# Kernel optimization log

Measured on AMD Instinct MI355X. Metric: run time of the kernel, lower is better.

Reference implementation:

```python
import jax, jax.numpy as jnp
import numpy as np

N_CODES = 1024
DIM = 64
COMMITMENT = 0.25


def setup_inputs() -> dict:
    key = jax.random.key(0)
    k1, k2 = jax.random.split(key)
    z = jax.random.normal(k1, (32, DIM, 64, 64), dtype=jnp.float32)
    # nn.Embedding weight initialized uniform(-1/n_codes, 1/n_codes)
    codebook = jax.random.uniform(
        k2, (N_CODES, DIM), dtype=jnp.float32,
        minval=-1.0 / N_CODES, maxval=1.0 / N_CODES)
    return {"z": z, "codebook": codebook}


def reference(z, codebook):
    B, C, H, W = z.shape
    # (B,C,H,W) -> (B*H*W, C)
    z_flat = jnp.transpose(z, (0, 2, 3, 1)).reshape(-1, C)
    # squared L2 distances via expansion: |z|^2 + |e|^2 - 2 z.e
    dists = (
        jnp.sum(z_flat ** 2, axis=1, keepdims=True)
        + jnp.sum(codebook ** 2, axis=1)
        - 2.0 * z_flat @ codebook.T
    )  # [N, n_codes]
    indices = jnp.argmin(dists, axis=1)  # [N]
    z_q = jnp.transpose(codebook[indices].reshape(B, H, W, C), (0, 3, 1, 2))
    commit_loss = jnp.mean((jax.lax.stop_gradient(z_q) - z) ** 2)
    codebook_loss = jnp.mean((z_q - jax.lax.stop_gradient(z)) ** 2)
    vq_loss = codebook_loss + COMMITMENT * commit_loss
    z_q_st = z + jax.lax.stop_gradient(z_q - z)  # straight-through
    return (z_q_st, vq_loss)
```

## Files before the change

### kernel.cpp

```cpp
#include <hip/hip_runtime.h>


constexpr int DIM    = 64;
constexpr int NCODES = 1024;
constexpr int HWSZ   = 4096;
constexpr int NPOS   = 131072;
constexpr int BLOCK  = 1024;
constexpr int PPB    = 512;
constexpr int GRID   = NPOS / PPB;
constexpr int CIP    = 68;

typedef float    f32x4  __attribute__((ext_vector_type(4)));
typedef float    f32x2  __attribute__((ext_vector_type(2)));
typedef unsigned uint2v __attribute__((ext_vector_type(2)));
typedef unsigned uint4v __attribute__((ext_vector_type(4)));

__global__ __launch_bounds__(BLOCK, 4) void vq_all(const float* __restrict__ z,
                                                   const float* __restrict__ cb,
                                                   float* __restrict__ out) {
    __shared__ __align__(16) unsigned char cb_lds[NCODES * DIM];
    __shared__ float cinit_lds[16 * CIP];
    __shared__ int   bj_lds[PPB];
    __shared__ float ls_lds[BLOCK / 64];

    const int tid  = threadIdx.x;
    const int w    = tid >> 6;
    const int lane = tid & 63;
    const int q    = lane >> 4;
    const int r    = lane & 15;
    const int p0   = blockIdx.x * PPB;
    const int b    = p0 >> 12;
    const int hwb  = p0 & 4095;

    {
        const int j = tid;
        const float4* src = (const float4*)(cb + (size_t)j * DIM);
        unsigned words[16];
        float nq = 0.f;
#pragma unroll
        for (int g8 = 0; g8 < 8; g8++) {
            float4 v0 = src[g8 * 2], v1 = src[g8 * 2 + 1];
            int lo = 0, hi = 0;
            lo = __builtin_amdgcn_cvt_pk_fp8_f32(v0.x * 512.f, v0.y * 512.f, lo, 0);
            lo = __builtin_amdgcn_cvt_pk_fp8_f32(v0.z * 512.f, v0.w * 512.f, lo, 1);
            hi = __builtin_amdgcn_cvt_pk_fp8_f32(v1.x * 512.f, v1.y * 512.f, hi, 0);
            hi = __builtin_amdgcn_cvt_pk_fp8_f32(v1.z * 512.f, v1.w * 512.f, hi, 1);
            words[g8 * 2] = (unsigned)lo; words[g8 * 2 + 1] = (unsigned)hi;
#pragma unroll
            for (int m = 0; m < 2; m++) {
                int wv = m ? hi : lo;
                f32x2 d0 = __builtin_amdgcn_cvt_pk_f32_fp8(wv, 0);
                f32x2 d1 = __builtin_amdgcn_cvt_pk_f32_fp8(wv, 1);
                nq += d0[0] * d0[0] + d0[1] * d0[1] + d1[0] * d1[0] + d1[1] * d1[1];
            }
        }
        const int sswz = (j & 3) ^ ((j >> 2) & 1);
#pragma unroll
        for (int u = 0; u < 4; u++) {
            int us = u ^ sswz;
            uint4v tq = {words[2 * u], words[2 * u + 1],
                         words[2 * u + 8], words[2 * u + 9]};
            *(uint4v*)&cb_lds[(size_t)j * 64 + us * 16] = tq;
        }
        cinit_lds[(j & 15) * CIP + (j >> 4)] = 8.f - nq * (1.f / 1024.f);
    }

    long  afrag[2][2];
    float zsq[2];
#pragma unroll
    for (int s = 0; s < 2; s++) {
        const float* zb = z + (size_t)b * DIM * HWSZ + hwb + s * 256 + w * 16 + r;
        float sq = 0.f;
#pragma unroll
        for (int h = 0; h < 2; h++) {
            float v[8];
#pragma unroll
            for (int i = 0; i < 8; i++) {
                v[i] = zb[(size_t)(h * 32 + q * 8 + i) * HWSZ];
                sq = fmaf(v[i], v[i], sq);
            }
            int lo = 0, hi = 0;
            lo = __builtin_amdgcn_cvt_pk_fp8_f32(v[0], v[1], lo, 0);
            lo = __builtin_amdgcn_cvt_pk_fp8_f32(v[2], v[3], lo, 1);
            hi = __builtin_amdgcn_cvt_pk_fp8_f32(v[4], v[5], hi, 0);
            hi = __builtin_amdgcn_cvt_pk_fp8_f32(v[6], v[7], hi, 1);
            uint2v u = {(unsigned)lo, (unsigned)hi};
            afrag[s][h] = __builtin_bit_cast(long, u);
        }
        sq += __shfl_xor(sq, 16, 64);
        sq += __shfl_xor(sq, 32, 64);
        zsq[s] = sq;
    }

    __syncthreads();

    const int bbase = r * 64 + ((q ^ (r & 3) ^ ((r >> 2) & 1)) * 16);

    float best0[4], best1[4], tmp0[4], tmp1[4];
#pragma unroll
    for (int g = 0; g < 4; g++) { best0[g] = 0.f; best1[g] = 0.f; }

    uint4v Bp[4];
    Bp[0] = *(const uint4v*)&cb_lds[0 * 1024 + bbase];
    Bp[1] = *(const uint4v*)&cb_lds[1 * 1024 + bbase];
    Bp[2] = *(const uint4v*)&cb_lds[2 * 1024 + bbase];
    Bp[3] = *(const uint4v*)&cb_lds[3 * 1024 + bbase];
    float4 ci[2];
    ci[0] = *(const float4*)&cinit_lds[r * CIP + 0];
    ci[1] = *(const float4*)&cinit_lds[r * CIP + 4];

    f32x4 accR[3][2];

    auto ISSUE = [&](int jt) {
        const int slot = jt & 3;
        const float cin = ci[(jt >> 2) & 1][jt & 3];
        uint2v blo = {Bp[slot][0], Bp[slot][1]};
        uint2v bhi = {Bp[slot][2], Bp[slot][3]};
        f32x4 c0 = {cin, cin, cin, cin};
        f32x4 a0 = __builtin_amdgcn_mfma_f32_16x16x32_fp8_fp8(
            afrag[0][0], __builtin_bit_cast(long, blo), c0, 0, 0, 0);
        a0 = __builtin_amdgcn_mfma_f32_16x16x32_fp8_fp8(
            afrag[0][1], __builtin_bit_cast(long, bhi), a0, 0, 0, 0);
        f32x4 a1 = __builtin_amdgcn_mfma_f32_16x16x32_fp8_fp8(
            afrag[1][0], __builtin_bit_cast(long, blo), c0, 0, 0, 0);
        a1 = __builtin_amdgcn_mfma_f32_16x16x32_fp8_fp8(
            afrag[1][1], __builtin_bit_cast(long, bhi), a1, 0, 0, 0);
        accR[jt % 3][0] = a0;
        accR[jt % 3][1] = a1;
        Bp[slot] = *(const uint4v*)&cb_lds[(((jt + 4) & 63) * 1024) + bbase];
        if ((jt & 3) == 3)
            ci[(jt >> 2) & 1] =
                *(const float4*)&cinit_lds[r * CIP + ((((jt >> 2) + 2) & 15) * 4)];
    };

    auto PROCESS = [&](int pj) {
        const unsigned kk  = (unsigned)(1023 - pj * 16);
        const unsigned tag = kk - (unsigned)r;
#pragma unroll
        for (int g = 0; g < 4; g++) {
            unsigned bits0 = (__float_as_uint(accR[pj % 3][0][g]) & ~1023u)
                           | (tag & 1023u);
            unsigned bits1 = (__float_as_uint(accR[pj % 3][1][g]) & ~1023u)
                           | (tag & 1023u);
            float pf0 = __uint_as_float(bits0);
            float pf1 = __uint_as_float(bits1);
            if ((pj & 1) == 0) {
                tmp0[g] = pf0; tmp1[g] = pf1;
            } else {
                best0[g] = fmaxf(fmaxf(best0[g], tmp0[g]), pf0);
                best1[g] = fmaxf(fmaxf(best1[g], tmp1[g]), pf1);
            }
        }
    };

    ISSUE(0);
    ISSUE(1);
#pragma unroll
    for (int jt = 2; jt < 64; jt++) {
        ISSUE(jt);
        PROCESS(jt - 2);
    }
    PROCESS(62);
    PROCESS(63);

    unsigned bestu0[4], bestu1[4];
#pragma unroll
    for (int g = 0; g < 4; g++) {
        unsigned v0 = __float_as_uint(best0[g]);
        unsigned v1 = __float_as_uint(best1[g]);
#pragma unroll
        for (int off = 1; off < 16; off <<= 1) {
            unsigned w0 = __shfl_xor((int)v0, off, 64);
            unsigned w1 = __shfl_xor((int)v1, off, 64);
            v0 = v0 > w0 ? v0 : w0;
            v1 = v1 > w1 ? v1 : w1;
        }
        bestu0[g] = v0; bestu1[g] = v1;
    }

    float lsum = 0.f;
    if (q == (r >> 2)) {
        int g = r & 3;
        unsigned v0 = bestu0[0], v1 = bestu1[0];
        v0 = (g == 1) ? bestu0[1] : v0;  v1 = (g == 1) ? bestu1[1] : v1;
        v0 = (g == 2) ? bestu0[2] : v0;  v1 = (g == 2) ? bestu1[2] : v1;
        v0 = (g == 3) ? bestu0[3] : v0;  v1 = (g == 3) ? bestu1[3] : v1;
        bj_lds[w * 16 + r]       = 1023 - (int)(v0 & 1023u);
        bj_lds[256 + w * 16 + r] = 1023 - (int)(v1 & 1023u);
        lsum = zsq[0] + (8.f - __uint_as_float(v0)) * (1.f / 256.f)
             + zsq[1] + (8.f - __uint_as_float(v1)) * (1.f / 256.f);
    }
#pragma unroll
    for (int off = 32; off > 0; off >>= 1) lsum += __shfl_down(lsum, off, 64);
    if (lane == 0) ls_lds[w] = lsum;
    __syncthreads();
    if (tid == 0) {
        float s = 0.f;
#pragma unroll
        for (int i = 0; i < BLOCK / 64; i++) s += ls_lds[i];
        atomicAdd(out + (size_t)NPOS * DIM, s * (1.25f / 8388608.f));
    }

    int posi = tid & 511;
    int uu   = tid >> 9;
    int myj  = bj_lds[posi];
    int swzj = (myj & 3) ^ ((myj >> 2) & 1);
    float* ob = out + (size_t)b * DIM * HWSZ + hwb + posi;
#pragma unroll
    for (int k = 0; k < 2; k++) {
        int u  = uu + 2 * k;
        int us = u ^ swzj;
        uint4v t = *(const uint4v*)&cb_lds[(size_t)myj * 64 + us * 16];
#pragma unroll
        for (int m = 0; m < 2; m++) {
            int cbase = (m == 0) ? (8 * u) : (32 + 8 * u);
#pragma unroll
            for (int wd = 0; wd < 2; wd++) {
                int word = (int)t[m * 2 + wd];
                f32x2 d0 = __builtin_amdgcn_cvt_pk_f32_fp8(word, 0);
                f32x2 d1 = __builtin_amdgcn_cvt_pk_f32_fp8(word, 1);
                ob[(size_t)(cbase + wd * 4 + 0) * HWSZ] = d0[0] * (1.f / 512.f);
                ob[(size_t)(cbase + wd * 4 + 1) * HWSZ] = d0[1] * (1.f / 512.f);
                ob[(size_t)(cbase + wd * 4 + 2) * HWSZ] = d1[0] * (1.f / 512.f);
                ob[(size_t)(cbase + wd * 4 + 3) * HWSZ] = d1[1] * (1.f / 512.f);
            }
        }
    }
}

extern "C" void kernel_launch(void* const* d_in, const int* in_sizes, int n_in,
                              void* d_out, int out_size, void* d_ws, size_t ws_size,
                              hipStream_t stream) {
    const float* z  = (const float*)d_in[0];
    const float* cb = (const float*)d_in[1];
    float* out = (float*)d_out;

    hipMemsetAsync(out + (size_t)NPOS * DIM, 0, sizeof(float), stream);
    vq_all<<<GRID, BLOCK, 0, stream>>>(z, cb, out);
}
```

Measured before the change: 105.5 us.

## Split codebook quantization into prep kernel and stream fp8 codebook from global

Codebook fp8 quantization and norm computation move into a separate prep kernel that writes a packed 64KB codebook and transposed init table to workspace. The main kernel no longer stages the codebook in LDS. It reads B fragments straight from global/L2 during the MFMA loop and uses smaller 256-thread blocks of 128 positions. This removes the per-block redundant quantization and the 64KB LDS footprint, which should raise occupancy. The cost is an extra launch and global-memory latency on the inner-loop operand loads.

```diff
diff --git a/kernel.cpp b/kernel.cpp
--- a/kernel.cpp
+++ b/kernel.cpp
@@ -5,21 +5,52 @@
 constexpr int NCODES = 1024;
 constexpr int HWSZ   = 4096;
 constexpr int NPOS   = 131072;
-constexpr int BLOCK  = 1024;
-constexpr int PPB    = 512;
+constexpr int BLOCK  = 256;
+constexpr int PPB    = 128;
 constexpr int GRID   = NPOS / PPB;
-constexpr int CIP    = 68;
 
 typedef float    f32x4  __attribute__((ext_vector_type(4)));
 typedef float    f32x2  __attribute__((ext_vector_type(2)));
 typedef unsigned uint2v __attribute__((ext_vector_type(2)));
 typedef unsigned uint4v __attribute__((ext_vector_type(4)));
 
-__global__ __launch_bounds__(BLOCK, 4) void vq_all(const float* __restrict__ z,
-                                                   const float* __restrict__ cb,
-                                                   float* __restrict__ out) {
-    __shared__ __align__(16) unsigned char cb_lds[NCODES * DIM];
-    __shared__ float cinit_lds[16 * CIP];
+__global__ __launch_bounds__(256) void vq_prep(const float* __restrict__ cb,
+                                               float* __restrict__ cinitT,
+                                               unsigned* __restrict__ cbq) {
+    int j = blockIdx.x * 256 + threadIdx.x;
+    const float4* src = (const float4*)(cb + (size_t)j * DIM);
+    unsigned words[16];
+    float nq = 0.f;
+#pragma unroll
+    for (int g8 = 0; g8 < 8; g8++) {
+        float4 v0 = src[g8 * 2], v1 = src[g8 * 2 + 1];
+        int lo = 0, hi = 0;
+        lo = __builtin_amdgcn_cvt_pk_fp8_f32(v0.x * 512.f, v0.y * 512.f, lo, 0);
+        lo = __builtin_amdgcn_cvt_pk_fp8_f32(v0.z * 512.f, v0.w * 512.f, lo, 1);
+        hi = __builtin_amdgcn_cvt_pk_fp8_f32(v1.x * 512.f, v1.y * 512.f, hi, 0);
+        hi = __builtin_amdgcn_cvt_pk_fp8_f32(v1.z * 512.f, v1.w * 512.f, hi, 1);
+        words[g8 * 2] = (unsigned)lo; words[g8 * 2 + 1] = (unsigned)hi;
+#pragma unroll
+        for (int m = 0; m < 2; m++) {
+            int wv = m ? hi : lo;
+            f32x2 d0 = __builtin_amdgcn_cvt_pk_f32_fp8(wv, 0);
+            f32x2 d1 = __builtin_amdgcn_cvt_pk_f32_fp8(wv, 1);
+            nq += d0[0] * d0[0] + d0[1] * d0[1] + d1[0] * d1[0] + d1[1] * d1[1];
+        }
+    }
+#pragma unroll
+    for (int u = 0; u < 4; u++) {
+        uint4v t = {words[2 * u], words[2 * u + 1],
+                    words[2 * u + 8], words[2 * u + 9]};
+        *(uint4v*)(cbq + (size_t)j * 16 + u * 4) = t;
+    }
+    cinitT[(j & 15) * 64 + (j >> 4)] = 8.f - nq * (1.f / 1024.f);
+}
+
+__global__ __launch_bounds__(BLOCK, 4) void vq_main(const float* __restrict__ z,
+                                                    const float* __restrict__ cinitT,
+                                                    const unsigned char* __restrict__ cbq,
+                                                    float* __restrict__ out) {
     __shared__ int   bj_lds[PPB];
     __shared__ float ls_lds[BLOCK / 64];
 
@@ -32,44 +63,11 @@
     const int b    = p0 >> 12;
     const int hwb  = p0 & 4095;
 
-    {
-        const int j = tid;
-        const float4* src = (const float4*)(cb + (size_t)j * DIM);
-        unsigned words[16];
-        float nq = 0.f;
-#pragma unroll
-        for (int g8 = 0; g8 < 8; g8++) {
-            float4 v0 = src[g8 * 2], v1 = src[g8 * 2 + 1];
-            int lo = 0, hi = 0;
-            lo = __builtin_amdgcn_cvt_pk_fp8_f32(v0.x * 512.f, v0.y * 512.f, lo, 0);
-            lo = __builtin_amdgcn_cvt_pk_fp8_f32(v0.z * 512.f, v0.w * 512.f, lo, 1);
-            hi = __builtin_amdgcn_cvt_pk_fp8_f32(v1.x * 512.f, v1.y * 512.f, hi, 0);
-            hi = __builtin_amdgcn_cvt_pk_fp8_f32(v1.z * 512.f, v1.w * 512.f, hi, 1);
-            words[g8 * 2] = (unsigned)lo; words[g8 * 2 + 1] = (unsigned)hi;
-#pragma unroll
-            for (int m = 0; m < 2; m++) {
-                int wv = m ? hi : lo;
-                f32x2 d0 = __builtin_amdgcn_cvt_pk_f32_fp8(wv, 0);
-                f32x2 d1 = __builtin_amdgcn_cvt_pk_f32_fp8(wv, 1);
-                nq += d0[0] * d0[0] + d0[1] * d0[1] + d1[0] * d1[0] + d1[1] * d1[1];
-            }
-        }
-        const int sswz = (j & 3) ^ ((j >> 2) & 1);
-#pragma unroll
-        for (int u = 0; u < 4; u++) {
-            int us = u ^ sswz;
-            uint4v tq = {words[2 * u], words[2 * u + 1],
-                         words[2 * u + 8], words[2 * u + 9]};
-            *(uint4v*)&cb_lds[(size_t)j * 64 + us * 16] = tq;
-        }
-        cinit_lds[(j & 15) * CIP + (j >> 4)] = 8.f - nq * (1.f / 1024.f);
-    }
-
     long  afrag[2][2];
     float zsq[2];
 #pragma unroll
     for (int s = 0; s < 2; s++) {
-        const float* zb = z + (size_t)b * DIM * HWSZ + hwb + s * 256 + w * 16 + r;
+        const float* zb = z + (size_t)b * DIM * HWSZ + hwb + w * 32 + s * 16 + r;
         float sq = 0.f;
 #pragma unroll
         for (int h = 0; h < 2; h++) {
@@ -92,22 +90,26 @@
         zsq[s] = sq;
     }
 
-    __syncthreads();
-
-    const int bbase = r * 64 + ((q ^ (r & 3) ^ ((r >> 2) & 1)) * 16);
+    const int bbase = r * 64 + q * 16;
+    const float* cip = cinitT + r * 64;
+
+    const unsigned char* bp0 = cbq + 0 * 1024 + bbase;
+    const unsigned char* bp1 = cbq + 1 * 1024 + bbase;
+    const unsigned char* bp2 = cbq + 2 * 1024 + bbase;
+    const unsigned char* bp3 = cbq + 3 * 1024 + bbase;
+
+    uint4v Bp[4];
+    Bp[0] = *(const uint4v*)bp0;  bp0 += 4096;
+    Bp[1] = *(const uint4v*)bp1;  bp1 += 4096;
+    Bp[2] = *(const uint4v*)bp2;  bp2 += 4096;
+    Bp[3] = *(const uint4v*)bp3;  bp3 += 4096;
+    float4 ci[2];
+    ci[0] = *(const float4*)(cip + 0);
+    ci[1] = *(const float4*)(cip + 4);
 
     float best0[4], best1[4], tmp0[4], tmp1[4];
 #pragma unroll
     for (int g = 0; g < 4; g++) { best0[g] = 0.f; best1[g] = 0.f; }
-
-    uint4v Bp[4];
-    Bp[0] = *(const uint4v*)&cb_lds[0 * 1024 + bbase];
-    Bp[1] = *(const uint4v*)&cb_lds[1 * 1024 + bbase];
-    Bp[2] = *(const uint4v*)&cb_lds[2 * 1024 + bbase];
-    Bp[3] = *(const uint4v*)&cb_lds[3 * 1024 + bbase];
-    float4 ci[2];
-    ci[0] = *(const float4*)&cinit_lds[r * CIP + 0];
-    ci[1] = *(const float4*)&cinit_lds[r * CIP + 4];
 
     f32x4 accR[3][2];
 
@@ -127,15 +129,17 @@
             afrag[1][1], __builtin_bit_cast(long, bhi), a1, 0, 0, 0);
         accR[jt % 3][0] = a0;
         accR[jt % 3][1] = a1;
-        Bp[slot] = *(const uint4v*)&cb_lds[(((jt + 4) & 63) * 1024) + bbase];
+        if (slot == 0)      { Bp[0] = *(const uint4v*)bp0;  bp0 += 4096; }
+        else if (slot == 1) { Bp[1] = *(const uint4v*)bp1;  bp1 += 4096; }
+        else if (slot == 2) { Bp[2] = *(const uint4v*)bp2;  bp2 += 4096; }
+        else                { Bp[3] = *(const uint4v*)bp3;  bp3 += 4096; }
         if ((jt & 3) == 3)
             ci[(jt >> 2) & 1] =
-                *(const float4*)&cinit_lds[r * CIP + ((((jt >> 2) + 2) & 15) * 4)];
+                *(const float4*)(cip + ((((jt >> 2) + 2) & 15) * 4));
     };
 
     auto PROCESS = [&](int pj) {
-        const unsigned kk  = (unsigned)(1023 - pj * 16);
-        const unsigned tag = kk - (unsigned)r;
+        const unsigned tag = (unsigned)(1023 - pj * 16) - (unsigned)r;
 #pragma unroll
         for (int g = 0; g < 4; g++) {
             unsigned bits0 = (__float_as_uint(accR[pj % 3][0][g]) & ~1023u)
@@ -185,8 +189,8 @@
         v0 = (g == 1) ? bestu0[1] : v0;  v1 = (g == 1) ? bestu1[1] : v1;
         v0 = (g == 2) ? bestu0[2] : v0;  v1 = (g == 2) ? bestu1[2] : v1;
         v0 = (g == 3) ? bestu0[3] : v0;  v1 = (g == 3) ? bestu1[3] : v1;
-        bj_lds[w * 16 + r]       = 1023 - (int)(v0 & 1023u);
-        bj_lds[256 + w * 16 + r] = 1023 - (int)(v1 & 1023u);
+        bj_lds[w * 32 + r]      = 1023 - (int)(v0 & 1023u);
+        bj_lds[w * 32 + 16 + r] = 1023 - (int)(v1 & 1023u);
         lsum = zsq[0] + (8.f - __uint_as_float(v0)) * (1.f / 256.f)
              + zsq[1] + (8.f - __uint_as_float(v1)) * (1.f / 256.f);
     }
@@ -195,22 +199,18 @@
     if (lane == 0) ls_lds[w] = lsum;
     __syncthreads();
     if (tid == 0) {
-        float s = 0.f;
-#pragma unroll
-        for (int i = 0; i < BLOCK / 64; i++) s += ls_lds[i];
+        float s = ls_lds[0] + ls_lds[1] + ls_lds[2] + ls_lds[3];
         atomicAdd(out + (size_t)NPOS * DIM, s * (1.25f / 8388608.f));
     }
 
-    int posi = tid & 511;
-    int uu   = tid >> 9;
+    int posi = tid & 127;
+    int uu   = tid >> 7;
     int myj  = bj_lds[posi];
-    int swzj = (myj & 3) ^ ((myj >> 2) & 1);
     float* ob = out + (size_t)b * DIM * HWSZ + hwb + posi;
 #pragma unroll
     for (int k = 0; k < 2; k++) {
         int u  = uu + 2 * k;
-        int us = u ^ swzj;
-        uint4v t = *(const uint4v*)&cb_lds[(size_t)myj * 64 + us * 16];
+        uint4v t = *(const uint4v*)(cbq + (size_t)myj * 64 + u * 16);
 #pragma unroll
         for (int m = 0; m < 2; m++) {
             int cbase = (m == 0) ? (8 * u) : (32 + 8 * u);
@@ -235,6 +235,11 @@
     const float* cb = (const float*)d_in[1];
     float* out = (float*)d_out;
 
+    float*    cinitT = (float*)d_ws;
+    unsigned* cbq    = (unsigned*)((char*)d_ws + 4096);
+
     hipMemsetAsync(out + (size_t)NPOS * DIM, 0, sizeof(float), stream);
-    vq_all<<<GRID, BLOCK, 0, stream>>>(z, cb, out);
+    vq_prep<<<NCODES / 256, 256, 0, stream>>>(cb, cinitT, cbq);
+    vq_main<<<GRID, BLOCK, 0, stream>>>(z, cinitT,
+                                        (const unsigned char*)cbq, out);
 }
```

Measured after the change: 116.7 us. +10.7%, slower.
